# Kernel tuning notes

Hardware: AMD Instinct MI355X
Metric: run time of the kernel (lower is better)

## Reference

```python
import jax, jax.numpy as jnp
import numpy as np

D_MODEL = 1024
NUM_HEADS = 16
D_K = D_MODEL // NUM_HEADS


def setup_inputs() -> dict:
    key = jax.random.key(0)
    ks = jax.random.split(key, 5)
    x = jax.random.normal(ks[0], (8, 1024, D_MODEL), dtype=jnp.float32)
    s_in = 1.0 / np.sqrt(D_MODEL)
    W_qkv = jax.random.normal(ks[1], (D_MODEL, 3 * D_MODEL), dtype=jnp.float32) * s_in
    b_qkv = jax.random.normal(ks[2], (3 * D_MODEL,), dtype=jnp.float32) * 0.01
    W_o = jax.random.normal(ks[3], (D_MODEL, D_MODEL), dtype=jnp.float32) * s_in
    b_o = jax.random.normal(ks[4], (D_MODEL,), dtype=jnp.float32) * 0.01
    return {"x": x, "W_qkv": W_qkv, "b_qkv": b_qkv, "W_o": W_o, "b_o": b_o}


def reference(x, W_qkv, b_qkv, W_o, b_o):
    B, N, D = x.shape
    qkv = x @ W_qkv + b_qkv                      # [B, N, 3D]
    qkv = qkv.reshape(B, N, 3, NUM_HEADS, D_K)
    qkv = jnp.transpose(qkv, (2, 0, 3, 1, 4))    # [3, B, H, N, d_k]
    q, k, v = qkv[0], qkv[1], qkv[2]
    scale = 1.0 / np.sqrt(D_K).astype(np.float32)
    attn = jnp.einsum('bhqd,bhkd->bhqk', q, k) * scale
    attn = jax.nn.softmax(attn, axis=-1)
    out = jnp.einsum('bhqk,bhkd->bhqd', attn, v)  # [B, H, N, d_k]
    out = jnp.transpose(out, (0, 2, 1, 3)).reshape(B, N, D)
    return out @ W_o + b_o
```

## Files before the change

kernel.cpp:

```cpp
#include <hip/hip_runtime.h>


typedef __attribute__((ext_vector_type(8))) short bf16x8;
typedef __attribute__((ext_vector_type(4))) float f32x4;

#define GLOAD_LDS16(gp, lp)                                                              \
  __builtin_amdgcn_global_load_lds((const __attribute__((address_space(1))) void*)(gp),  \
                                   (__attribute__((address_space(3))) void*)(lp), 16, 0, 0)

__device__ __forceinline__ unsigned short f2bf(float f) {
  unsigned int u = __float_as_uint(f);
  u += 0x7fffu + ((u >> 16) & 1u);
  return (unsigned short)(u >> 16);
}

__global__ __launch_bounds__(256) void cast_f32_to_bf16(
    const float* __restrict__ in, unsigned short* __restrict__ out, int n4) {
  int stride = gridDim.x * blockDim.x;
  for (int i = blockIdx.x * blockDim.x + threadIdx.x; i < n4; i += stride) {
    float4 v = reinterpret_cast<const float4*>(in)[i];
    ushort4 o;
    o.x = f2bf(v.x); o.y = f2bf(v.y); o.z = f2bf(v.z); o.w = f2bf(v.w);
    reinterpret_cast<ushort4*>(out)[i] = o;
  }
}

__global__ __launch_bounds__(256) void transpose_cast(
    const float* __restrict__ W, unsigned short* __restrict__ Wt, int R, int C) {
  __shared__ float tile[32][33];
  int tx = threadIdx.x & 31, ty = threadIdx.x >> 5;
  int c0 = blockIdx.x * 32, r0 = blockIdx.y * 32;
  #pragma unroll
  for (int i = 0; i < 4; i++) {
    int r = r0 + ty + i * 8;
    tile[ty + i * 8][tx] = W[(size_t)r * C + c0 + tx];
  }
  __syncthreads();
  #pragma unroll
  for (int i = 0; i < 4; i++) {
    int c = c0 + ty + i * 8;
    Wt[(size_t)c * R + r0 + tx] = f2bf(tile[tx][ty + i * 8]);
  }
}

template <int MODE>
__global__ __launch_bounds__(256) void gemm_bf16(
    const unsigned short* __restrict__ A, const unsigned short* __restrict__ Bt,
    const float* __restrict__ bias, unsigned short* __restrict__ qkv_out,
    float* __restrict__ Cout) {
  __shared__ __align__(16) unsigned short As[2][128 * 32];
  __shared__ __align__(16) unsigned short Bs[2][128 * 32];
  const int t = threadIdx.x;
  const int lane = t & 63, wid = t >> 6;
  const int lr = lane & 15, g = lane >> 4;
  const int row0 = blockIdx.y * 128, col0 = blockIdx.x * 128;
  const int wr = wid >> 1, wc = wid & 1;

  auto stage = [&](int buf, int kt) {
    #pragma unroll
    for (int s = 0; s < 2; s++) {
      int o = wid * 1024 + s * 4096;
      int ol = o + lane * 16;
      int row = ol >> 6;
      int ch = ((ol >> 4) & 3) ^ ((row >> 1) & 3);
      const unsigned short* ga = A + (size_t)(row0 + row) * 1024 + kt * 32 + ch * 8;
      GLOAD_LDS16(ga, (char*)&As[buf][0] + o);
      const unsigned short* gb = Bt + (size_t)(col0 + row) * 1024 + kt * 32 + ch * 8;
      GLOAD_LDS16(gb, (char*)&Bs[buf][0] + o);
    }
  };

  f32x4 acc[4][4] = {};
  stage(0, 0);
  int buf = 0;
  for (int kt = 0; kt < 32; kt++) {
    __syncthreads();
    if (kt + 1 < 32) stage(buf ^ 1, kt + 1);
    bf16x8 a[4], b[4];
    #pragma unroll
    for (int m = 0; m < 4; m++) {
      int row = wr * 64 + m * 16 + lr;
      a[m] = *(const bf16x8*)((const char*)&As[buf][0] + row * 64 +
                              ((g ^ ((row >> 1) & 3)) * 16));
    }
    #pragma unroll
    for (int n = 0; n < 4; n++) {
      int col = wc * 64 + n * 16 + lr;
      b[n] = *(const bf16x8*)((const char*)&Bs[buf][0] + col * 64 +
                              ((g ^ ((col >> 1) & 3)) * 16));
    }
    #pragma unroll
    for (int m = 0; m < 4; m++)
      #pragma unroll
      for (int n = 0; n < 4; n++)
        acc[m][n] = __builtin_amdgcn_mfma_f32_16x16x32_bf16(a[m], b[n], acc[m][n], 0, 0, 0);
    buf ^= 1;
  }

  if (MODE == 0) {
    const int which = col0 >> 10;
    if (which == 2) {
      #pragma unroll
      for (int m = 0; m < 4; m++) {
        int row = row0 + wr * 64 + m * 16 + g * 4;
        int bb = row >> 10, nn = row & 1023;
        #pragma unroll
        for (int n = 0; n < 4; n++) {
          int col = col0 + wc * 64 + n * 16 + lr;
          int cc = col & 1023;
          int h = cc >> 6, dk = cc & 63;
          float bv = bias[col];
          ushort4 w;
          w.x = f2bf(acc[m][n][0] + bv);
          w.y = f2bf(acc[m][n][1] + bv);
          w.z = f2bf(acc[m][n][2] + bv);
          w.w = f2bf(acc[m][n][3] + bv);
          size_t idx = ((size_t)2 << 23) + (((size_t)(bb * 16 + h)) << 16) +
                       (size_t)dk * 1024 + nn;
          *(ushort4*)(qkv_out + idx) = w;
        }
      }
    } else {
      #pragma unroll
      for (int m = 0; m < 4; m++) {
        #pragma unroll
        for (int n = 0; n < 4; n++) {
          int col = col0 + wc * 64 + n * 16 + lr;
          int cc = col & 1023;
          int h = cc >> 6, dk = cc & 63;
          #pragma unroll
          for (int r = 0; r < 4; r++) {
            int row = row0 + wr * 64 + m * 16 + g * 4 + r;
            int bb = row >> 10, nn = row & 1023;
            float v = acc[m][n][r] + bias[col];
            if (which == 0) v *= 0.125f;
            size_t idx = ((size_t)which << 23) +
                         (((size_t)((bb * 16 + h) * 1024 + nn)) << 6) + dk;
            qkv_out[idx] = f2bf(v);
          }
        }
      }
    }
  } else {
    #pragma unroll
    for (int m = 0; m < 4; m++) {
      #pragma unroll
      for (int n = 0; n < 4; n++) {
        int col = col0 + wc * 64 + n * 16 + lr;
        #pragma unroll
        for (int r = 0; r < 4; r++) {
          int row = row0 + wr * 64 + m * 16 + g * 4 + r;
          Cout[(size_t)row * 1024 + col] = acc[m][n][r] + bias[col];
        }
      }
    }
  }
}

__global__ __launch_bounds__(512) void attn_mfma(
    const unsigned short* __restrict__ qkv, unsigned short* __restrict__ attn_out) {
  __shared__ __align__(16) unsigned short K_lds[2][64 * 64];
  __shared__ __align__(16) unsigned short V_lds[2][64 * 64];
  __shared__ __align__(16) unsigned short P_lds[128 * 64];

  const int bid = ((blockIdx.x & 7) << 7) + (blockIdx.x >> 3);
  const int bh = bid >> 3, qt = bid & 7;
  const unsigned short* Qp = qkv + ((size_t)bh << 16);
  const unsigned short* Kp = qkv + (1u << 23) + ((size_t)bh << 16);
  const unsigned short* Vt = qkv + (2u << 23) + ((size_t)bh << 16);

  const int t = threadIdx.x;
  const int lane = t & 63, wid = t >> 6;
  const int lr = lane & 15, g = lane >> 4;

  bf16x8 qf[2];
  {
    int qrow = qt * 128 + wid * 16 + lr;
    qf[0] = *(const bf16x8*)(Qp + (size_t)qrow * 64 + g * 8);
    qf[1] = *(const bf16x8*)(Qp + (size_t)qrow * 64 + 32 + g * 8);
  }

  const int srow = t >> 3;
  const int sch  = (t & 7) ^ (srow & 7);
  const int so   = t * 16;

  auto stage = [&](int buf, int kt) {
    GLOAD_LDS16(Kp + (size_t)(kt * 64 + srow) * 64 + sch * 8, (char*)&K_lds[buf][0] + so);
    GLOAD_LDS16(Vt + (size_t)srow * 1024 + kt * 64 + sch * 8, (char*)&V_lds[buf][0] + so);
  };

  f32x4 o_acc[4] = {};
  float den[4] = {0.f, 0.f, 0.f, 0.f};

  stage(0, 0);
  __syncthreads();
  int buf = 0;
  for (int kt = 0; kt < 16; kt++) {
    if (kt + 1 < 16) stage(buf ^ 1, kt + 1);

    f32x4 s4[4] = {};
    __builtin_amdgcn_s_setprio(1);
    #pragma unroll
    for (int ks = 0; ks < 4; ks++) {
      int krow = ks * 16 + lr;
      #pragma unroll
      for (int c = 0; c < 2; c++) {
        bf16x8 kf = *(const bf16x8*)((char*)&K_lds[buf][0] + krow * 128 +
                                     ((c * 64 + g * 16) ^ ((krow & 7) << 4)));
        s4[ks] = __builtin_amdgcn_mfma_f32_16x16x32_bf16(qf[c], kf, s4[ks], 0, 0, 0);
      }
    }
    __builtin_amdgcn_s_setprio(0);

    #pragma unroll
    for (int ks = 0; ks < 4; ks++) {
      #pragma unroll
      for (int r = 0; r < 4; r++) {
        float e = __expf(s4[ks][r]);
        den[r] += e;
        int q = wid * 16 + g * 4 + r;
        *(unsigned short*)((char*)P_lds + q * 128 +
                           (((ks * 16 + lr) * 2) ^ ((q & 7) << 4))) = f2bf(e);
      }
    }

    bf16x8 pa[2];
    {
      int q = wid * 16 + lr;
      #pragma unroll
      for (int c = 0; c < 2; c++)
        pa[c] = *(const bf16x8*)((char*)P_lds + q * 128 +
                                 ((c * 64 + g * 16) ^ ((q & 7) << 4)));
    }
    __builtin_amdgcn_s_setprio(1);
    #pragma unroll
    for (int ds_ = 0; ds_ < 4; ds_++) {
      int drow = ds_ * 16 + lr;
      #pragma unroll
      for (int c = 0; c < 2; c++) {
        bf16x8 vf = *(const bf16x8*)((char*)&V_lds[buf][0] + drow * 128 +
                                     ((c * 64 + g * 16) ^ ((drow & 7) << 4)));
        o_acc[ds_] = __builtin_amdgcn_mfma_f32_16x16x32_bf16(pa[c], vf, o_acc[ds_], 0, 0, 0);
      }
    }
    __builtin_amdgcn_s_setprio(0);
    __syncthreads();
    buf ^= 1;
  }

  #pragma unroll
  for (int r = 0; r < 4; r++) {
    den[r] += __shfl_xor(den[r], 1, 64);
    den[r] += __shfl_xor(den[r], 2, 64);
    den[r] += __shfl_xor(den[r], 4, 64);
    den[r] += __shfl_xor(den[r], 8, 64);
  }

  const int bb = bh >> 4, h = bh & 15;
  #pragma unroll
  for (int ds_ = 0; ds_ < 4; ds_++) {
    #pragma unroll
    for (int r = 0; r < 4; r++) {
      int q = qt * 128 + wid * 16 + g * 4 + r;
      int d = h * 64 + ds_ * 16 + lr;
      attn_out[((size_t)(bb * 1024 + q)) * 1024 + d] = f2bf(o_acc[ds_][r] / den[r]);
    }
  }
}

extern "C" void kernel_launch(void* const* d_in, const int* in_sizes, int n_in,
                              void* d_out, int out_size, void* d_ws, size_t ws_size,
                              hipStream_t stream) {
  const float* x     = (const float*)d_in[0];
  const float* W_qkv = (const float*)d_in[1];
  const float* b_qkv = (const float*)d_in[2];
  const float* W_o   = (const float*)d_in[3];
  const float* b_o   = (const float*)d_in[4];
  float* out = (float*)d_out;

  unsigned short* ws      = (unsigned short*)d_ws;
  unsigned short* x_bf    = ws;
  unsigned short* wqkv_t  = x_bf + 8388608;
  unsigned short* wo_t    = wqkv_t + 3145728;
  unsigned short* qkv     = wo_t + 1048576;
  unsigned short* attn_o  = qkv + 25165824;

  cast_f32_to_bf16<<<2048, 256, 0, stream>>>(x, x_bf, 8388608 / 4);
  transpose_cast<<<dim3(96, 32), 256, 0, stream>>>(W_qkv, wqkv_t, 1024, 3072);
  transpose_cast<<<dim3(32, 32), 256, 0, stream>>>(W_o, wo_t, 1024, 1024);

  gemm_bf16<0><<<dim3(24, 64), 256, 0, stream>>>(x_bf, wqkv_t, b_qkv, qkv, nullptr);
  attn_mfma<<<1024, 512, 0, stream>>>(qkv, attn_o);
  gemm_bf16<1><<<dim3(8, 64), 256, 0, stream>>>(attn_o, wo_t, b_o, nullptr, out);
}
```

Measured before the change: 189.0 us.

## Enlarge GEMM tiles to 256x128x64 with interleaved async loads and MFMA phases

The bf16 GEMM is rebuilt around 256x128 output tiles with a K-step of 64 and 512 threads (8 waves). Global-to-LDS loads for the next stage are split into chunks issued between MFMA phases, with explicit vmcnt waits, barriers and s_setprio so memory traffic overlaps compute. An 8-way XOR swizzle avoids LDS bank conflicts. The intent is more reuse per load and better latency hiding, at the cost of more LDS, halved grid size and many extra barriers.

```diff
diff --git a/kernel.cpp b/kernel.cpp
--- a/kernel.cpp
+++ b/kernel.cpp
@@ -44,57 +44,110 @@
 }
 
 template <int MODE>
-__global__ __launch_bounds__(256) void gemm_bf16(
+__global__ __launch_bounds__(512) void gemm256(
     const unsigned short* __restrict__ A, const unsigned short* __restrict__ Bt,
     const float* __restrict__ bias, unsigned short* __restrict__ qkv_out,
     float* __restrict__ Cout) {
-  __shared__ __align__(16) unsigned short As[2][128 * 32];
-  __shared__ __align__(16) unsigned short Bs[2][128 * 32];
+  __shared__ __align__(16) unsigned short As[2][256 * 64];
+  __shared__ __align__(16) unsigned short Bs[2][128 * 64];
   const int t = threadIdx.x;
   const int lane = t & 63, wid = t >> 6;
   const int lr = lane & 15, g = lane >> 4;
-  const int row0 = blockIdx.y * 128, col0 = blockIdx.x * 128;
+  const int row0 = blockIdx.y * 256, col0 = blockIdx.x * 128;
   const int wr = wid >> 1, wc = wid & 1;
-
-  auto stage = [&](int buf, int kt) {
-    #pragma unroll
-    for (int s = 0; s < 2; s++) {
-      int o = wid * 1024 + s * 4096;
-      int ol = o + lane * 16;
-      int row = ol >> 6;
-      int ch = ((ol >> 4) & 3) ^ ((row >> 1) & 3);
-      const unsigned short* ga = A + (size_t)(row0 + row) * 1024 + kt * 32 + ch * 8;
-      GLOAD_LDS16(ga, (char*)&As[buf][0] + o);
-      const unsigned short* gb = Bt + (size_t)(col0 + row) * 1024 + kt * 32 + ch * 8;
-      GLOAD_LDS16(gb, (char*)&Bs[buf][0] + o);
-    }
+  const int srow = t >> 3, sch = t & 7;
+
+  auto stA = [&](int buf, int kt, int j) {
+    int row = j * 64 + srow;
+    int ch = sch ^ (row & 7);
+    GLOAD_LDS16(A + (size_t)(row0 + row) * 1024 + kt * 64 + ch * 8,
+                (char*)&As[buf][0] + j * 8192 + t * 16);
+  };
+  auto stB = [&](int buf, int kt, int j) {
+    int row = j * 64 + srow;
+    int ch = sch ^ (row & 7);
+    GLOAD_LDS16(Bt + (size_t)(col0 + row) * 1024 + kt * 64 + ch * 8,
+                (char*)&Bs[buf][0] + j * 8192 + t * 16);
+  };
+  auto rdA = [&](int buf, int c, int m) -> bf16x8 {
+    int r = wr * 64 + m * 16 + lr;
+    return *(const bf16x8*)((const char*)&As[buf][0] + r * 128 +
+                            ((c * 64 + g * 16) ^ ((r & 7) << 4)));
+  };
+  auto rdB = [&](int buf, int c, int n) -> bf16x8 {
+    int r = wc * 64 + n * 16 + lr;
+    return *(const bf16x8*)((const char*)&Bs[buf][0] + r * 128 +
+                            ((c * 64 + g * 16) ^ ((r & 7) << 4)));
   };
 
   f32x4 acc[4][4] = {};
-  stage(0, 0);
-  int buf = 0;
-  for (int kt = 0; kt < 32; kt++) {
-    __syncthreads();
-    if (kt + 1 < 32) stage(buf ^ 1, kt + 1);
-    bf16x8 a[4], b[4];
-    #pragma unroll
-    for (int m = 0; m < 4; m++) {
-      int row = wr * 64 + m * 16 + lr;
-      a[m] = *(const bf16x8*)((const char*)&As[buf][0] + row * 64 +
-                              ((g ^ ((row >> 1) & 3)) * 16));
-    }
-    #pragma unroll
-    for (int n = 0; n < 4; n++) {
-      int col = wc * 64 + n * 16 + lr;
-      b[n] = *(const bf16x8*)((const char*)&Bs[buf][0] + col * 64 +
-                              ((g ^ ((col >> 1) & 3)) * 16));
-    }
-    #pragma unroll
-    for (int m = 0; m < 4; m++)
+
+  stA(0, 0, 0); stA(0, 0, 1); stA(0, 0, 2); stA(0, 0, 3);
+  stB(0, 0, 0); stB(0, 0, 1);
+
+  for (int kt = 0; kt < 16; kt++) {
+    const int buf = kt & 1;
+    const bool pf = (kt + 1 < 16);
+    if (pf) {
+      stA(buf ^ 1, kt + 1, 0); stA(buf ^ 1, kt + 1, 1);
+      asm volatile("s_waitcnt vmcnt(2)" ::: "memory");
+    } else {
+      asm volatile("s_waitcnt vmcnt(0)" ::: "memory");
+    }
+    __builtin_amdgcn_s_barrier();
+
+    bf16x8 b0[4], b1[4], afr[2];
+
+    #pragma unroll
+    for (int n = 0; n < 4; n++) b0[n] = rdB(buf, 0, n);
+    afr[0] = rdA(buf, 0, 0); afr[1] = rdA(buf, 0, 1);
+    if (pf) { stA(buf ^ 1, kt + 1, 2); stA(buf ^ 1, kt + 1, 3); }
+    __builtin_amdgcn_s_barrier();
+    __builtin_amdgcn_s_setprio(1);
+    #pragma unroll
+    for (int m = 0; m < 2; m++)
       #pragma unroll
       for (int n = 0; n < 4; n++)
-        acc[m][n] = __builtin_amdgcn_mfma_f32_16x16x32_bf16(a[m], b[n], acc[m][n], 0, 0, 0);
-    buf ^= 1;
+        acc[m][n] = __builtin_amdgcn_mfma_f32_16x16x32_bf16(afr[m], b0[n], acc[m][n], 0, 0, 0);
+    __builtin_amdgcn_s_setprio(0);
+    __builtin_amdgcn_s_barrier();
+
+    afr[0] = rdA(buf, 0, 2); afr[1] = rdA(buf, 0, 3);
+    if (pf) { stB(buf ^ 1, kt + 1, 0); stB(buf ^ 1, kt + 1, 1); }
+    __builtin_amdgcn_s_barrier();
+    __builtin_amdgcn_s_setprio(1);
+    #pragma unroll
+    for (int m = 0; m < 2; m++)
+      #pragma unroll
+      for (int n = 0; n < 4; n++)
+        acc[2 + m][n] = __builtin_amdgcn_mfma_f32_16x16x32_bf16(afr[m], b0[n], acc[2 + m][n], 0, 0, 0);
+    __builtin_amdgcn_s_setprio(0);
+    __builtin_amdgcn_s_barrier();
+
+    #pragma unroll
+    for (int n = 0; n < 4; n++) b1[n] = rdB(buf, 1, n);
+    afr[0] = rdA(buf, 1, 0); afr[1] = rdA(buf, 1, 1);
+    __builtin_amdgcn_s_barrier();
+    __builtin_amdgcn_s_setprio(1);
+    #pragma unroll
+    for (int m = 0; m < 2; m++)
+      #pragma unroll
+      for (int n = 0; n < 4; n++)
+        acc[m][n] = __builtin_amdgcn_mfma_f32_16x16x32_bf16(afr[m], b1[n], acc[m][n], 0, 0, 0);
+    __builtin_amdgcn_s_setprio(0);
+    __builtin_amdgcn_s_barrier();
+
+    afr[0] = rdA(buf, 1, 2); afr[1] = rdA(buf, 1, 3);
+    __builtin_amdgcn_s_barrier();
+    __builtin_amdgcn_s_setprio(1);
+    #pragma unroll
+    for (int m = 0; m < 2; m++)
+      #pragma unroll
+      for (int n = 0; n < 4; n++)
+        acc[2 + m][n] = __builtin_amdgcn_mfma_f32_16x16x32_bf16(afr[m], b1[n], acc[2 + m][n], 0, 0, 0);
+    __builtin_amdgcn_s_setprio(0);
+    asm volatile("" ::: "memory");
+    __builtin_amdgcn_s_barrier();
   }
 
   if (MODE == 0) {
@@ -289,7 +342,7 @@
   transpose_cast<<<dim3(96, 32), 256, 0, stream>>>(W_qkv, wqkv_t, 1024, 3072);
   transpose_cast<<<dim3(32, 32), 256, 0, stream>>>(W_o, wo_t, 1024, 1024);
 
-  gemm_bf16<0><<<dim3(24, 64), 256, 0, stream>>>(x_bf, wqkv_t, b_qkv, qkv, nullptr);
+  gemm256<0><<<dim3(24, 32), 512, 0, stream>>>(x_bf, wqkv_t, b_qkv, qkv, nullptr);
   attn_mfma<<<1024, 512, 0, stream>>>(qkv, attn_o);
-  gemm_bf16<1><<<dim3(8, 64), 256, 0, stream>>>(attn_o, wo_t, b_o, nullptr, out);
-}
+  gemm256<1><<<dim3(8, 32), 512, 0, stream>>>(attn_o, wo_t, b_o, nullptr, out);
+}
```

After: 192.5 us. No clear change (+1.8%).
